# Kernel optimization log

Measured on AMD Instinct MI355X. Metric: run time of the kernel, lower is better.

## Reference

```python
import jax, jax.numpy as jnp
import numpy as np

N, D, V = 16384, 2048, 8192  # rows, code bits, val_range (codebook size)


def setup_inputs() -> dict:
    key = jax.random.key(0)
    k1, k2 = jax.random.split(key)
    x = jax.random.normal(k1, (N, D), dtype=jnp.float32)   # encoded rows
    di = jax.random.normal(k2, (D, V), dtype=jnp.float32)  # decode codebook (fwd.di)
    return {"x": x, "di": di}


def reference(x, di):
    # Original loops over rows doing (1,D)@(D,V) then argmax; batched this is one
    # GEMM [N,D]@[D,V] -> [N,V] followed by argmax over the V axis, cast to float32
    # (the torch code stores the index into a float32 output tensor).
    scores = jnp.matmul(x, di)                  # [N, V]
    return jnp.argmax(scores, axis=1).astype(jnp.float32)  # [N]
```

## Files before the change

### kernel.cpp

```cpp
#include <hip/hip_runtime.h>

typedef _Float16 f16x8 __attribute__((ext_vector_type(8)));
typedef float f32x4 __attribute__((ext_vector_type(4)));

__device__ __forceinline__ unsigned int fkey(float f) {
    unsigned int u = __float_as_uint(f);
    return u ^ ((u & 0x80000000u) ? 0xFFFFFFFFu : 0x80000000u);
}
__device__ __forceinline__ float unkey(unsigned int k) {
    unsigned int u = (k & 0x80000000u) ? (k ^ 0x80000000u) : ~k;
    return __uint_as_float(u);
}

__device__ __forceinline__ unsigned int f32_to_e4m3(float f) {
    float a = fabsf(f);
    a = fminf(a, 448.0f);
    unsigned int s = (__float_as_uint(f) >> 24) & 0x80u;
    if (a < 0.015625f) {
        int m = (int)rintf(a * 512.0f);
        return s | (unsigned int)m;
    }
    int e = ilogbf(a);
    float step = ldexpf(1.0f, e - 3);
    int q = (int)rintf(a / step);
    if (q == 16) { e += 1; q = 8; }
    return s | (unsigned int)(((e + 7) << 3) | (q - 8));
}

__global__ __launch_bounds__(256) void prep_x_q(
    const float* __restrict__ x, unsigned char* __restrict__ Xq)
{
    size_t base = ((size_t)blockIdx.x * 256 + threadIdx.x) * 8;
    float4 a0 = *(const float4*)(x + base);
    float4 a1 = *(const float4*)(x + base + 4);
    float v[8] = {a0.x, a0.y, a0.z, a0.w, a1.x, a1.y, a1.z, a1.w};
    unsigned long long b = 0;
#pragma unroll
    for (int j = 0; j < 8; ++j)
        b |= (unsigned long long)f32_to_e4m3(v[j]) << (8 * j);
    *(unsigned long long*)(Xq + base) = b;
}

__global__ __launch_bounds__(256) void prep_di_q(
    const float* __restrict__ di, unsigned char* __restrict__ DqT,
    _Float16* __restrict__ DhT, _Float16* __restrict__ DlT, int D, int V)
{
    int v  = blockIdx.x * 64 + (threadIdx.x & 63);
    int d0 = blockIdx.y * 32 + (threadIdx.x >> 6) * 8;
    f16x8 h, l;
    unsigned long long b = 0;
#pragma unroll
    for (int j = 0; j < 8; ++j) {
        float val = di[(size_t)(d0 + j) * V + v];
        _Float16 hh = (_Float16)val;
        h[j] = hh;
        l[j] = (_Float16)(val - (float)hh);
        b |= (unsigned long long)f32_to_e4m3(val) << (8 * j);
    }
    *(unsigned long long*)(DqT + (size_t)v * D + d0) = b;
    *(f16x8*)(DhT + (size_t)v * D + d0) = h;
    *(f16x8*)(DlT + (size_t)v * D + d0) = l;
}

__global__ __launch_bounds__(512, 1) void gemm_fp8_top2(
    const unsigned char* __restrict__ Xq, const unsigned char* __restrict__ DqT,
    unsigned long long* __restrict__ cand, int N, int D, int V)
{
    __shared__ __align__(16) unsigned char sm[65536];

    const int tid = threadIdx.x;
    const int w = tid >> 6, lane = tid & 63;
    const int wr = w >> 2, wc = w & 3;
    const int lm = lane & 15, lg = lane >> 4;
    const int rch = lane >> 4;
    const int sl  = lane & 15;

    const int cpx = gridDim.x >> 3;
    const int swz = (blockIdx.x & 7) * cpx + (blockIdx.x >> 3);
    const int bm = (swz >> 5) * 256;
    const int bn = (swz & 31) * 256;

    auto stage = [&](int buf, int k0) {
#pragma unroll
        for (int i = 0; i < 16; ++i) {
            const int g = w * 16 + i;
            const int op = g >> 6;
            const int cc = g & 63;
            const int row = cc * 4 + rch;
            const int slog = (sl >> 1) ^ (row & 7);
            const unsigned char* src =
                (op ? DqT + (size_t)(bn + row) * D : Xq + (size_t)(bm + row) * D)
                + k0 + slog * 8 + (sl & 1) * 4;
            __builtin_amdgcn_global_load_lds(
                (const __attribute__((address_space(1))) void*)src,
                (__attribute__((address_space(3))) void*)
                    (sm + buf * 32768 + op * 16384 + cc * 256),
                4, 0, 0);
        }
    };
    auto lda = [&](int buf, int op, int row, int kk) -> long {
        return *(const long*)(sm + buf * 32768 + op * 16384 + row * 64 +
                              (((kk << 2) | lg) ^ (lm & 7)) * 8);
    };

    f32x4 acc[8][4];
#pragma unroll
    for (int fm = 0; fm < 8; ++fm)
#pragma unroll
        for (int fn = 0; fn < 4; ++fn) acc[fm][fn] = (f32x4){0.f, 0.f, 0.f, 0.f};

    const int nt = D / 64;
    int cb = 0;

    stage(0, 0);
    __syncthreads();

#pragma unroll 1
    for (int t = 0; t < nt; ++t) {
        if (t + 1 < nt) stage(cb ^ 1, (t + 1) * 64);
#pragma unroll
        for (int kk = 0; kk < 2; ++kk) {
            long bfr[4];
#pragma unroll
            for (int fn = 0; fn < 4; ++fn)
                bfr[fn] = lda(cb, 1, wc * 64 + fn * 16 + lm, kk);
#pragma unroll
            for (int fm = 0; fm < 8; ++fm) {
                long a = lda(cb, 0, wr * 128 + fm * 16 + lm, kk);
#pragma unroll
                for (int fn = 0; fn < 4; ++fn)
                    acc[fm][fn] = __builtin_amdgcn_mfma_f32_16x16x32_fp8_fp8(
                        a, bfr[fn], acc[fm][fn], 0, 0, 0);
            }
        }
        __syncthreads();
        cb ^= 1;
    }

    const int nblk = V >> 8;
    const int blkn = bn >> 8;
#pragma unroll
    for (int fm = 0; fm < 8; ++fm)
#pragma unroll
        for (int j = 0; j < 4; ++j) {
            unsigned long long p[4];
#pragma unroll
            for (int fn = 0; fn < 4; ++fn) {
                const int col = bn + wc * 64 + fn * 16 + lm;
                p[fn] = ((unsigned long long)fkey(acc[fm][fn][j]) << 32) |
                        (unsigned long long)(0xFFFFFFFFu - (unsigned int)col);
            }
            unsigned long long t1 = p[0] > p[1] ? p[0] : p[1];
            unsigned long long t2 = p[0] > p[1] ? p[1] : p[0];
#pragma unroll
            for (int fn = 2; fn < 4; ++fn) {
                if (p[fn] > t1) { t2 = t1; t1 = p[fn]; }
                else if (p[fn] > t2) t2 = p[fn];
            }
#pragma unroll
            for (int m = 1; m < 16; m <<= 1) {
                unsigned long long o1 = __shfl_xor(t1, m, 16);
                unsigned long long o2 = __shfl_xor(t2, m, 16);
                unsigned long long n1 = t1 > o1 ? t1 : o1;
                unsigned long long lo = t1 > o1 ? o1 : t1;
                unsigned long long m2 = t2 > o2 ? t2 : o2;
                t2 = lo > m2 ? lo : m2;
                t1 = n1;
            }
            if (lm == 0) {
                const int row = bm + wr * 128 + fm * 16 + lg * 4 + j;
                size_t ci = (((size_t)row * nblk + blkn) * 4 + wc) * 2;
                cand[ci] = t1;
                cand[ci + 1] = t2;
            }
        }
}

#define DELTA 16.5f

__global__ __launch_bounds__(256) void refine_kernel(
    const unsigned long long* __restrict__ cand,
    const float* __restrict__ X,
    const _Float16* __restrict__ DhT, const _Float16* __restrict__ DlT,
    float* __restrict__ out, int N, int D, int V)
{
    const int w = threadIdx.x >> 6, lane = threadIdx.x & 63;
    const int r = blockIdx.x * 4 + w;
    if (r >= N) return;

    const int nent = (V >> 8) * 8;
    const unsigned long long* cr = cand + (size_t)r * nent;

    unsigned long long p[4];
#pragma unroll
    for (int i = 0; i < 4; ++i) p[i] = cr[lane * 4 + i];

    unsigned long long pmax = p[0];
#pragma unroll
    for (int i = 1; i < 4; ++i) if (p[i] > pmax) pmax = p[i];
#pragma unroll
    for (int m = 1; m < 64; m <<= 1) {
        unsigned long long o = __shfl_xor(pmax, m);
        if (o > pmax) pmax = o;
    }

    const float s1 = unkey((unsigned int)(pmax >> 32));
    const unsigned int kthr = fkey(s1 - DELTA);

    int cnt = 0;
    unsigned long long masks[4];
#pragma unroll
    for (int i = 0; i < 4; ++i) {
        masks[i] = __ballot((unsigned int)(p[i] >> 32) >= kthr);
        cnt += __popcll(masks[i]);
    }

    if (cnt <= 1) {
        if (lane == 0)
            out[r] = (float)(0xFFFFFFFFu - (unsigned int)(pmax & 0xFFFFFFFFull));
        return;
    }

    const float* xrow = X + (size_t)r * D;
    float xbuf[32];
#pragma unroll
    for (int q = 0; q < 8; ++q) {
        float4 xv = *(const float4*)(xrow + lane * 32 + q * 4);
        xbuf[q * 4 + 0] = xv.x; xbuf[q * 4 + 1] = xv.y;
        xbuf[q * 4 + 2] = xv.z; xbuf[q * 4 + 3] = xv.w;
    }

    unsigned long long bestp = 0;
    for (int i = 0; i < 4; ++i) {
        unsigned long long mask = masks[i];
        while (mask) {
            const int src = __ffsll((unsigned long long)mask) - 1;
            mask &= mask - 1;
            const unsigned long long cp = __shfl(p[i], src);
            const int col = (int)(0xFFFFFFFFu - (unsigned int)(cp & 0xFFFFFFFFull));

            const f16x8* dh = (const f16x8*)(DhT + (size_t)col * D) + lane * 4;
            const f16x8* dl = (const f16x8*)(DlT + (size_t)col * D) + lane * 4;
            float s = 0.0f;
#pragma unroll
            for (int q = 0; q < 4; ++q) {
                f16x8 h = dh[q], l = dl[q];
#pragma unroll
                for (int e = 0; e < 8; ++e)
                    s = fmaf(xbuf[q * 8 + e], (float)h[e] + (float)l[e], s);
            }
#pragma unroll
            for (int m = 1; m < 64; m <<= 1) s += __shfl_xor(s, m);

            const unsigned long long pp =
                ((unsigned long long)fkey(s) << 32) |
                (unsigned long long)(0xFFFFFFFFu - (unsigned int)col);
            if (pp > bestp) bestp = pp;
        }
    }
    if (lane == 0)
        out[r] = (float)(0xFFFFFFFFu - (unsigned int)(bestp & 0xFFFFFFFFull));
}

#define FBK 16
#define FTM 8
#define FTN 8

__global__ __launch_bounds__(256) void gemm_argmax_fp32_kernel(
    const float* __restrict__ A, const float* __restrict__ B,
    unsigned long long* __restrict__ best, int N, int D, int V)
{
    __shared__ float As[FBK][128 + 4];
    __shared__ float Bs[FBK][128 + 4];

    const int tid = threadIdx.x;
    const int tx = tid & 15;
    const int ty = tid >> 4;
    const int bm = blockIdx.y * 128;
    const int bn = blockIdx.x * 128;

    const int arow  = tid >> 2;
    const int acol4 = tid & 3;
    const int brow  = tid >> 5;
    const int bcol4 = tid & 31;

    float acc[FTM][FTN];
#pragma unroll
    for (int i = 0; i < FTM; ++i)
#pragma unroll
        for (int j = 0; j < FTN; ++j) acc[i][j] = 0.0f;

    for (int k0 = 0; k0 < D; k0 += FBK) {
        float4 a0 = *reinterpret_cast<const float4*>(&A[(size_t)(bm + arow) * D + k0 + acol4 * 4]);
        float4 a1 = *reinterpret_cast<const float4*>(&A[(size_t)(bm + arow + 64) * D + k0 + acol4 * 4]);
        float4 b0 = *reinterpret_cast<const float4*>(&B[(size_t)(k0 + brow) * V + bn + bcol4 * 4]);
        float4 b1 = *reinterpret_cast<const float4*>(&B[(size_t)(k0 + brow + 8) * V + bn + bcol4 * 4]);

        As[acol4 * 4 + 0][arow] = a0.x;
        As[acol4 * 4 + 1][arow] = a0.y;
        As[acol4 * 4 + 2][arow] = a0.z;
        As[acol4 * 4 + 3][arow] = a0.w;
        As[acol4 * 4 + 0][arow + 64] = a1.x;
        As[acol4 * 4 + 1][arow + 64] = a1.y;
        As[acol4 * 4 + 2][arow + 64] = a1.z;
        As[acol4 * 4 + 3][arow + 64] = a1.w;
        *reinterpret_cast<float4*>(&Bs[brow][bcol4 * 4]) = b0;
        *reinterpret_cast<float4*>(&Bs[brow + 8][bcol4 * 4]) = b1;

        __syncthreads();
#pragma unroll
        for (int kk = 0; kk < FBK; ++kk) {
            float4 av0 = *reinterpret_cast<const float4*>(&As[kk][ty * FTM]);
            float4 av1 = *reinterpret_cast<const float4*>(&As[kk][ty * FTM + 4]);
            float4 bv0 = *reinterpret_cast<const float4*>(&Bs[kk][tx * FTN]);
            float4 bv1 = *reinterpret_cast<const float4*>(&Bs[kk][tx * FTN + 4]);
            float a[FTM] = {av0.x, av0.y, av0.z, av0.w, av1.x, av1.y, av1.z, av1.w};
            float b[FTN] = {bv0.x, bv0.y, bv0.z, bv0.w, bv1.x, bv1.y, bv1.z, bv1.w};
#pragma unroll
            for (int i = 0; i < FTM; ++i)
#pragma unroll
                for (int j = 0; j < FTN; ++j)
                    acc[i][j] = fmaf(a[i], b[j], acc[i][j]);
        }
        __syncthreads();
    }

#pragma unroll
    for (int i = 0; i < FTM; ++i) {
        float bv = acc[i][0];
        int bc = bn + tx * FTN;
#pragma unroll
        for (int j = 1; j < FTN; ++j) {
            float v = acc[i][j];
            int c = bn + tx * FTN + j;
            if (v > bv) { bv = v; bc = c; }
        }
        unsigned long long packed =
            ((unsigned long long)fkey(bv) << 32) |
            (unsigned long long)(0xFFFFFFFFu - (unsigned int)bc);
#pragma unroll
        for (int m = 1; m < 16; m <<= 1) {
            unsigned long long o = __shfl_xor(packed, m, 16);
            if (o > packed) packed = o;
        }
        if (tx == 0) atomicMax(&best[bm + ty * FTM + i], packed);
    }
}

__global__ void decode_kernel(const unsigned long long* __restrict__ best,
                              float* __restrict__ out, int N)
{
    int i = blockIdx.x * blockDim.x + threadIdx.x;
    if (i < N) {
        unsigned int inv = (unsigned int)(best[i] & 0xFFFFFFFFull);
        out[i] = (float)(0xFFFFFFFFu - inv);
    }
}

extern "C" void kernel_launch(void* const* d_in, const int* in_sizes, int n_in,
                              void* d_out, int out_size, void* d_ws, size_t ws_size,
                              hipStream_t stream) {
    const float* A = (const float*)d_in[0];
    const float* B = (const float*)d_in[1];
    float* out = (float*)d_out;

    const int N = out_size;
    const int D = in_sizes[0] / N;
    const int V = in_sizes[1] / D;

    const size_t szXq = (size_t)N * D;
    const size_t szDq = (size_t)D * V;
    const size_t szDh = (size_t)D * V * sizeof(_Float16);
    const size_t candsz = (size_t)N * (V / 256) * 4 * 2 * 8;
    const size_t need = szXq + szDq + 2 * szDh + candsz;

    if (ws_size >= need) {
        char* wsp = (char*)d_ws;
        unsigned char* Xq  = (unsigned char*)(wsp);
        unsigned char* DqT = (unsigned char*)(wsp + szXq);
        _Float16* DhT = (_Float16*)(wsp + szXq + szDq);
        _Float16* DlT = (_Float16*)(wsp + szXq + szDq + szDh);
        unsigned long long* cand =
            (unsigned long long*)(wsp + szXq + szDq + 2 * szDh);

        prep_x_q<<<(int)(((size_t)N * D) / (256 * 8)), 256, 0, stream>>>(A, Xq);
        prep_di_q<<<dim3(V / 64, D / 32), 256, 0, stream>>>(B, DqT, DhT, DlT, D, V);
        gemm_fp8_top2<<<(N / 256) * (V / 256), 512, 0, stream>>>(
            Xq, DqT, cand, N, D, V);
        refine_kernel<<<(N + 3) / 4, 256, 0, stream>>>(
            cand, A, DhT, DlT, out, N, D, V);
    } else {
        unsigned long long* best = (unsigned long long*)d_ws;
        hipMemsetAsync(best, 0, (size_t)N * sizeof(unsigned long long), stream);
        gemm_argmax_fp32_kernel<<<dim3(V / 128, N / 128), 256, 0, stream>>>(A, B, best, N, D, V);
        decode_kernel<<<(N + 255) / 256, 256, 0, stream>>>(best, out, N);
    }
}
```

Before: 701.6 us.

## Switch FP8 GEMM to scaled 32x32x64 MFMA with 16-byte LDS staging

Replaces the 16x16x32 FP8 MFMA with the gfx950 scaled 32x32x64 f8f6f4 MFMA using unit scales. The LDS staging moves from 4-byte to 16-byte global_load_lds transfers, with a new swizzle and 32-byte fragment reads. The top-2 epilogue is rewritten for the 32x32 accumulator layout. The aim is higher matrix-core throughput and fewer load instructions. The risks are correctness of the new fragment and accumulator layouts and LDS bank conflicts under the new swizzle.

```diff
diff --git a/kernel.cpp b/kernel.cpp
--- a/kernel.cpp
+++ b/kernel.cpp
@@ -2,6 +2,9 @@
 
 typedef _Float16 f16x8 __attribute__((ext_vector_type(8)));
 typedef float f32x4 __attribute__((ext_vector_type(4)));
+typedef float f32x16 __attribute__((ext_vector_type(16)));
+typedef int i32x4 __attribute__((ext_vector_type(4)));
+typedef int i32x8 __attribute__((ext_vector_type(8)));
 
 __device__ __forceinline__ unsigned int fkey(float f) {
     unsigned int u = __float_as_uint(f);
@@ -62,7 +65,7 @@
     *(f16x8*)(DlT + (size_t)v * D + d0) = l;
 }
 
-__global__ __launch_bounds__(512, 1) void gemm_fp8_top2(
+__global__ __launch_bounds__(512, 1) void gemm_mx_top2(
     const unsigned char* __restrict__ Xq, const unsigned char* __restrict__ DqT,
     unsigned long long* __restrict__ cand, int N, int D, int V)
 {
@@ -71,43 +74,49 @@
     const int tid = threadIdx.x;
     const int w = tid >> 6, lane = tid & 63;
     const int wr = w >> 2, wc = w & 3;
-    const int lm = lane & 15, lg = lane >> 4;
-    const int rch = lane >> 4;
-    const int sl  = lane & 15;
+    const int l31 = lane & 31, hl = lane >> 5;
 
     const int cpx = gridDim.x >> 3;
     const int swz = (blockIdx.x & 7) * cpx + (blockIdx.x >> 3);
     const int bm = (swz >> 5) * 256;
     const int bn = (swz & 31) * 256;
 
+    const int srow_in = lane >> 2;
+    const int sp      = lane & 3;
     auto stage = [&](int buf, int k0) {
 #pragma unroll
-        for (int i = 0; i < 16; ++i) {
-            const int g = w * 16 + i;
-            const int op = g >> 6;
-            const int cc = g & 63;
-            const int row = cc * 4 + rch;
-            const int slog = (sl >> 1) ^ (row & 7);
+        for (int i = 0; i < 4; ++i) {
+            const int g = w * 4 + i;
+            const int op = g >> 4;
+            const int c  = g & 15;
+            const int row = c * 16 + srow_in;
+            const int slog = sp ^ ((row >> 1) & 3);
             const unsigned char* src =
                 (op ? DqT + (size_t)(bn + row) * D : Xq + (size_t)(bm + row) * D)
-                + k0 + slog * 8 + (sl & 1) * 4;
+                + k0 + slog * 16;
             __builtin_amdgcn_global_load_lds(
                 (const __attribute__((address_space(1))) void*)src,
                 (__attribute__((address_space(3))) void*)
-                    (sm + buf * 32768 + op * 16384 + cc * 256),
-                4, 0, 0);
+                    (sm + buf * 32768 + op * 16384 + c * 1024),
+                16, 0, 0);
         }
     };
-    auto lda = [&](int buf, int op, int row, int kk) -> long {
-        return *(const long*)(sm + buf * 32768 + op * 16384 + row * 64 +
-                              (((kk << 2) | lg) ^ (lm & 7)) * 8);
+    auto ldfrag = [&](int buf, int op, int r) -> i32x8 {
+        const unsigned char* base =
+            sm + buf * 32768 + op * 16384 + (r >> 4) * 1024 + (r & 15) * 64;
+        const int sw = (r >> 1) & 3;
+        i32x4 lo = *(const i32x4*)(base + (((hl << 1)    ) ^ sw) * 16);
+        i32x4 hi = *(const i32x4*)(base + (((hl << 1) | 1) ^ sw) * 16);
+        return __builtin_shufflevector(lo, hi, 0, 1, 2, 3, 4, 5, 6, 7);
     };
 
-    f32x4 acc[8][4];
-#pragma unroll
-    for (int fm = 0; fm < 8; ++fm)
-#pragma unroll
-        for (int fn = 0; fn < 4; ++fn) acc[fm][fn] = (f32x4){0.f, 0.f, 0.f, 0.f};
+    f32x16 acc[4][2];
+#pragma unroll
+    for (int fm = 0; fm < 4; ++fm)
+#pragma unroll
+        for (int fn = 0; fn < 2; ++fn)
+#pragma unroll
+            for (int q = 0; q < 16; ++q) acc[fm][fn][q] = 0.0f;
 
     const int nt = D / 64;
     int cb = 0;
@@ -118,20 +127,16 @@
 #pragma unroll 1
     for (int t = 0; t < nt; ++t) {
         if (t + 1 < nt) stage(cb ^ 1, (t + 1) * 64);
-#pragma unroll
-        for (int kk = 0; kk < 2; ++kk) {
-            long bfr[4];
-#pragma unroll
-            for (int fn = 0; fn < 4; ++fn)
-                bfr[fn] = lda(cb, 1, wc * 64 + fn * 16 + lm, kk);
-#pragma unroll
-            for (int fm = 0; fm < 8; ++fm) {
-                long a = lda(cb, 0, wr * 128 + fm * 16 + lm, kk);
-#pragma unroll
-                for (int fn = 0; fn < 4; ++fn)
-                    acc[fm][fn] = __builtin_amdgcn_mfma_f32_16x16x32_fp8_fp8(
-                        a, bfr[fn], acc[fm][fn], 0, 0, 0);
-            }
+
+        i32x8 b0 = ldfrag(cb, 1, wc * 64 + 0 * 32 + l31);
+        i32x8 b1 = ldfrag(cb, 1, wc * 64 + 1 * 32 + l31);
+#pragma unroll
+        for (int fm = 0; fm < 4; ++fm) {
+            i32x8 a = ldfrag(cb, 0, wr * 128 + fm * 32 + l31);
+            acc[fm][0] = __builtin_amdgcn_mfma_scale_f32_32x32x64_f8f6f4(
+                a, b0, acc[fm][0], 0, 0, 0, 0x7F7F7F7F, 0, 0x7F7F7F7F);
+            acc[fm][1] = __builtin_amdgcn_mfma_scale_f32_32x32x64_f8f6f4(
+                a, b1, acc[fm][1], 0, 0, 0, 0x7F7F7F7F, 0, 0x7F7F7F7F);
         }
         __syncthreads();
         cb ^= 1;
@@ -140,35 +145,30 @@
     const int nblk = V >> 8;
     const int blkn = bn >> 8;
 #pragma unroll
-    for (int fm = 0; fm < 8; ++fm)
-#pragma unroll
-        for (int j = 0; j < 4; ++j) {
-            unsigned long long p[4];
-#pragma unroll
-            for (int fn = 0; fn < 4; ++fn) {
-                const int col = bn + wc * 64 + fn * 16 + lm;
-                p[fn] = ((unsigned long long)fkey(acc[fm][fn][j]) << 32) |
-                        (unsigned long long)(0xFFFFFFFFu - (unsigned int)col);
-            }
-            unsigned long long t1 = p[0] > p[1] ? p[0] : p[1];
-            unsigned long long t2 = p[0] > p[1] ? p[1] : p[0];
-#pragma unroll
-            for (int fn = 2; fn < 4; ++fn) {
-                if (p[fn] > t1) { t2 = t1; t1 = p[fn]; }
-                else if (p[fn] > t2) t2 = p[fn];
-            }
-#pragma unroll
-            for (int m = 1; m < 16; m <<= 1) {
-                unsigned long long o1 = __shfl_xor(t1, m, 16);
-                unsigned long long o2 = __shfl_xor(t2, m, 16);
+    for (int fm = 0; fm < 4; ++fm)
+#pragma unroll
+        for (int j = 0; j < 16; ++j) {
+            const int row = bm + wr * 128 + fm * 32 + (j & 3) + 8 * (j >> 2) + 4 * hl;
+            const int c0 = bn + wc * 64 + l31;
+            unsigned long long p0 =
+                ((unsigned long long)fkey(acc[fm][0][j]) << 32) |
+                (unsigned long long)(0xFFFFFFFFu - (unsigned int)c0);
+            unsigned long long p1 =
+                ((unsigned long long)fkey(acc[fm][1][j]) << 32) |
+                (unsigned long long)(0xFFFFFFFFu - (unsigned int)(c0 + 32));
+            unsigned long long t1 = p0 > p1 ? p0 : p1;
+            unsigned long long t2 = p0 > p1 ? p1 : p0;
+#pragma unroll
+            for (int m = 1; m < 32; m <<= 1) {
+                unsigned long long o1 = __shfl_xor(t1, m);
+                unsigned long long o2 = __shfl_xor(t2, m);
                 unsigned long long n1 = t1 > o1 ? t1 : o1;
                 unsigned long long lo = t1 > o1 ? o1 : t1;
                 unsigned long long m2 = t2 > o2 ? t2 : o2;
                 t2 = lo > m2 ? lo : m2;
                 t1 = n1;
             }
-            if (lm == 0) {
-                const int row = bm + wr * 128 + fm * 16 + lg * 4 + j;
+            if (l31 == 0) {
                 size_t ci = (((size_t)row * nblk + blkn) * 4 + wc) * 2;
                 cand[ci] = t1;
                 cand[ci + 1] = t2;
@@ -385,7 +385,7 @@
 
         prep_x_q<<<(int)(((size_t)N * D) / (256 * 8)), 256, 0, stream>>>(A, Xq);
         prep_di_q<<<dim3(V / 64, D / 32), 256, 0, stream>>>(B, DqT, DhT, DlT, D, V);
-        gemm_fp8_top2<<<(N / 256) * (V / 256), 512, 0, stream>>>(
+        gemm_mx_top2<<<(N / 256) * (V / 256), 512, 0, stream>>>(
             Xq, DqT, cand, N, D, V);
         refine_kernel<<<(N + 3) / 4, 256, 0, stream>>>(
             cand, A, DhT, DlT, out, N, D, V);
```

New measurement: 737.4 us. 1.05x slower.
